# Optimization experiments

Hardware: AMD Instinct MI355X
Metric: run time of the kernel (lower is better)

Reference implementation:

```python
import jax, jax.numpy as jnp
import numpy as np

H = 128
W = 128
DELTA = 7000.0  # sigmainv in the original (delta default 7000)


def setup_inputs() -> dict:
    key = jax.random.key(0)
    k1, k2, k3, k4 = jax.random.split(key, 4)
    B, P, F, TH, TW = 2, 300, 512, 512, 512
    points_bxpx3 = jax.random.uniform(k1, (B, P, 3), jnp.float32) * 2.0 - 1.0  # NDC cube [-1,1]
    faces_fx3 = jax.random.randint(k2, (F, 3), 0, P, dtype=jnp.int32)
    uv_bxpx2 = jax.random.uniform(k3, (B, P, 2), jnp.float32)  # texcoords in [0,1]
    texture_bx3xthxtw = jax.random.uniform(k4, (B, 3, TH, TW), jnp.float32)
    return {"points_bxpx3": points_bxpx3, "faces_fx3": faces_fx3,
            "uv_bxpx2": uv_bxpx2, "texture_bx3xthxtw": texture_bx3xthxtw}


def _edge(ax, ay, bx, by, px, py):
    # signed area * 2 of triangle (a, b, p); standard edge function
    return (bx - ax) * (py - ay) - (by - ay) * (px - ax)


def _seg_d2(ax, ay, bx, by, px, py):
    # squared distance from point p to segment (a, b)
    abx, aby = bx - ax, by - ay
    apx, apy = px - ax, py - ay
    denom = abx * abx + aby * aby + 1e-12
    t = jnp.clip((apx * abx + apy * aby) / denom, 0.0, 1.0)
    dx = apx - t * abx
    dy = apy - t * aby
    return dx * dx + dy * dy


def _rasterize(points_bxpx3, faces_fx3, feats_bxfx3xd, height, width, delta):
    """Soft DIB-R-style rasterizer.
    Returns (imfeat [B,H,W,D], improb [B,H,W,1]).
    """
    B = points_bxpx3.shape[0]
    v = points_bxpx3[:, faces_fx3]                      # (B,F,3,3) gathered face vertices
    x0, x1, x2 = (v[:, :, i, 0][:, :, None, None] for i in range(3))
    y0, y1, y2 = (v[:, :, i, 1][:, :, None, None] for i in range(3))
    z0, z1, z2 = (v[:, :, i, 2][:, :, None, None] for i in range(3))

    # pixel-center grid in NDC; y flipped (top row = +1)
    px = ((jnp.arange(width, dtype=points_bxpx3.dtype) + 0.5) / width * 2.0 - 1.0)[None, None, None, :]
    py = (1.0 - (jnp.arange(height, dtype=points_bxpx3.dtype) + 0.5) / height * 2.0)[None, None, :, None]

    area = _edge(x0, y0, x1, y1, x2, y2)                # (B,F,1,1) == normal_z (cross-product z)
    front = area > 1e-8                                  # front-facing (normalz > 0) cull
    inv_area = 1.0 / jnp.where(front, area, 1.0)

    w0 = _edge(x1, y1, x2, y2, px, py) * inv_area        # (B,F,H,W) barycentrics
    w1 = _edge(x2, y2, x0, y0, px, py) * inv_area
    w2 = _edge(x0, y0, x1, y1, px, py) * inv_area
    inside = front & (w0 >= 0) & (w1 >= 0) & (w2 >= 0)

    z_pix = w0 * z0 + w1 * z1 + w2 * z2                  # interpolated depth
    zbuf = jnp.where(inside, z_pix, -1e9)
    best = jnp.argmax(zbuf, axis=1)                      # (B,H,W) nearest covering face
    hit = jnp.any(inside, axis=1)[..., None].astype(points_bxpx3.dtype)  # (B,H,W,1)

    # gather winning barycentrics and per-face vertex features
    w = jnp.stack([w0, w1, w2], axis=-1)                 # (B,F,H,W,3)
    idx = jnp.broadcast_to(best[:, None, :, :, None], (B, 1, height, width, 3))
    wb = jnp.take_along_axis(w, idx, axis=1)[:, 0]       # (B,H,W,3)
    fb = jax.vmap(lambda f, i: f[i])(feats_bxfx3xd, best)  # (B,H,W,3,D)
    imfeat = jnp.einsum('bhwk,bhwkd->bhwd', wb, fb) * hit

    # soft coverage: prob of each face = exp(-delta * d2(pixel, triangle)); z-buffer blend
    d2 = jnp.minimum(
        jnp.minimum(_seg_d2(x0, y0, x1, y1, px, py), _seg_d2(x1, y1, x2, y2, px, py)),
        _seg_d2(x2, y2, x0, y0, px, py))
    d2 = jnp.where(inside, 0.0, d2)
    p = jnp.where(front, jnp.exp(-delta * d2), 0.0)      # (B,F,H,W)
    log_miss = jnp.sum(jnp.log1p(-jnp.clip(p, 0.0, 1.0 - 1e-7)), axis=1)  # (B,H,W)
    improb = (1.0 - jnp.exp(log_miss))[..., None]
    return imfeat, improb


def _fragmentshader(imtexcoords, texture_bx3xthxtw, hardmask):
    # bilinear texture sampling; background is zero
    B, C, TH, TW = texture_bx3xthxtw.shape
    u = jnp.clip(imtexcoords[..., 0], 0.0, 1.0)
    vv = jnp.clip(imtexcoords[..., 1], 0.0, 1.0)
    fx = u * (TW - 1)
    fy = (1.0 - vv) * (TH - 1)
    x0 = jnp.floor(fx).astype(jnp.int32); x1 = jnp.minimum(x0 + 1, TW - 1)
    y0 = jnp.floor(fy).astype(jnp.int32); y1 = jnp.minimum(y0 + 1, TH - 1)
    wx = (fx - x0)[:, None]; wy = (fy - y0)[:, None]     # (B,1,H,W)

    def g(tex, yy, xx):  # tex (C,TH,TW), yy/xx (H,W) -> (C,H,W)
        return tex[:, yy, xx]
    c00 = jax.vmap(g)(texture_bx3xthxtw, y0, x0)
    c01 = jax.vmap(g)(texture_bx3xthxtw, y0, x1)
    c10 = jax.vmap(g)(texture_bx3xthxtw, y1, x0)
    c11 = jax.vmap(g)(texture_bx3xthxtw, y1, x1)
    col = (c00 * (1 - wx) * (1 - wy) + c01 * wx * (1 - wy)
           + c10 * (1 - wx) * wy + c11 * wx * wy)        # (B,C,H,W)
    return col.transpose(0, 2, 3, 1) * hardmask          # (B,H,W,C)


def reference(points_bxpx3, faces_fx3, uv_bxpx2, texture_bx3xthxtw):
    # texture mode: per-face vertex features = [u, v, mask=1]
    uvf = uv_bxpx2[:, faces_fx3]                          # (B,F,3,2)
    ones = jnp.ones_like(uvf[..., :1])
    feats = jnp.concatenate([uvf, ones], axis=-1)         # (B,F,3,3)
    imfeat, improb = _rasterize(points_bxpx3, faces_fx3, feats, H, W, DELTA)
    imtexcoords = imfeat[..., :2]
    hardmask = jax.lax.stop_gradient(imfeat[..., 2:3])    # .detach() in the original
    imrender = _fragmentshader(imtexcoords, texture_bx3xthxtw, hardmask)
    return imrender, improb
```

## Files before the change

### kernel.cpp

```cpp
#include <hip/hip_runtime.h>
#include <math.h>

constexpr int kB = 2, kP = 300, kF = 512, kH = 128, kW = 128, kTH = 512, kTW = 512;
constexpr float kDelta = 7000.0f;
constexpr float kCut = 0.0363f;
constexpr float kThr2 = 0.012928f;
constexpr float kLogInside = -15.9423847f;

__device__ __forceinline__ unsigned zmap(float f) {
    unsigned b = __float_as_uint(f);
    return (b & 0x80000000u) ? ~b : (b | 0x80000000u);
}

__global__ __launch_bounds__(512, 8) void render_all(const float* __restrict__ pts,
                                                     const int* __restrict__ faces,
                                                     const float* __restrict__ uvs,
                                                     const float* __restrict__ tex,
                                                     float* __restrict__ out) {
    __shared__ float4 sA[kF], sB[kF], sC[kF];
    __shared__ float4 sV[kF];
    __shared__ ushort4 s_j3[kF];
    __shared__ float s_uv[kP * 2];
    __shared__ unsigned long long s_best[64];
    __shared__ float s_lm[64];
    __shared__ int s_wsum[8];
    float4* s_pxW = sA;
    int4* s_pxO = (int4*)(sA + 64);

    int tile = (int)blockIdx.x;
    int b = tile >> 8;
    int rem = tile & 255;
    int ty = rem >> 4, tx = rem & 15;
    int tid = (int)threadIdx.x;
    int lane = tid & 63;
    int wv = tid >> 6;

    {
        int f = tid;
        int i0 = faces[f * 3 + 0], i1 = faces[f * 3 + 1], i2 = faces[f * 3 + 2];
        const float* pb = pts + b * kP * 3;
        float x0 = pb[i0 * 3], y0 = pb[i0 * 3 + 1], z0 = pb[i0 * 3 + 2];
        float x1 = pb[i1 * 3], y1 = pb[i1 * 3 + 1], z1 = pb[i1 * 3 + 2];
        float x2 = pb[i2 * 3], y2 = pb[i2 * 3 + 1], z2 = pb[i2 * 3 + 2];
        float area = (x1 - x0) * (y2 - y0) - (y1 - y0) * (x2 - x0);
        bool front = area > 1e-8f;

        const float* gu = uvs + b * (kP * 2);
        for (int i = tid; i < kP * 2; i += 512) s_uv[i] = gu[i];
        if (tid < 64) { s_best[tid] = 0ull; s_lm[tid] = 0.0f; }
        sA[f] = make_float4(0.0f, 0.0f, -1e30f, 0.0f);
        sB[f] = make_float4(0.0f, -1e30f, 0.0f, 0.0f);
        sC[f] = make_float4(-1e30f, 0.0f, 0.0f, 0.0f);
        sV[f] = make_float4(1e15f, 1e15f, 1e15f, 1e15f);
        unsigned long long bal = __ballot(front);
        if (lane == 0) s_wsum[wv] = __popcll(bal);
        __syncthreads();

        int base = 0;
#pragma unroll
        for (int w = 0; w < 8; ++w) base += (w < wv) ? s_wsum[w] : 0;
        int k = base + __popcll(bal & ((1ull << lane) - 1ull));

        if (front) {
            int slot = ((k & 7) << 6) | (k >> 3);
            float inv_a = 1.0f / area;
            float e0x = x2 - x1, e0y = y2 - y1;
            float e1x = x0 - x2, e1y = y0 - y2;
            float e2x = x1 - x0, e2y = y1 - y0;
            float l0 = fmaf(e0x, e0x, e0y * e0y);
            float l1 = fmaf(e1x, e1x, e1y * e1y);
            float l2 = fmaf(e2x, e2x, e2y * e2y);
            float s0 = rsqrtf(l0 + 1e-12f);
            float s1 = rsqrtf(l1 + 1e-12f);
            float s2 = rsqrtf(l2 + 1e-12f);
            float A0 = -e0y * s0, B0 = e0x * s0, C0 = (e0y * x1 - e0x * y1) * s0;
            float A1 = -e1y * s1, B1 = e1x * s1, C1 = (e1y * x2 - e1x * y2) * s1;
            float A2 = -e2y * s2, B2 = e2x * s2, C2 = (e2y * x0 - e2x * y0) * s2;
            float a0 = -e0y * inv_a, b0 = e0x * inv_a, c0 = (e0y * x1 - e0x * y1) * inv_a;
            float a1 = -e1y * inv_a, b1 = e1x * inv_a, c1 = (e1y * x2 - e1x * y2) * inv_a;
            float a2 = -e2y * inv_a, b2 = e2x * inv_a, c2 = (e2y * x0 - e2x * y0) * inv_a;
            sA[slot] = make_float4(A0, B0, C0, A1);
            sB[slot] = make_float4(B1, C1, A2, B2);
            sC[slot] = make_float4(C2,
                                   a0 * z0 + a1 * z1 + a2 * z2,
                                   b0 * z0 + b1 * z1 + b2 * z2,
                                   c0 * z0 + c1 * z1 + c2 * z2);
            sV[slot] = make_float4(x0, y0, x1, y1);
            s_j3[slot] = make_ushort4((unsigned short)i0, (unsigned short)i1,
                                      (unsigned short)i2, 0);
        }
    }
    __syncthreads();

    int pyi = ty * 8 + (lane >> 3);
    int pxi = tx * 8 + (lane & 7);
    float px = ((float)pxi + 0.5f) * (2.0f / 128.0f) - 1.0f;
    float py = 1.0f - ((float)pyi + 0.5f) * (2.0f / 128.0f);

    float cx = (float)(tx * 8 + 4) * (2.0f / 128.0f) - 1.0f;
    float cy = 1.0f - (float)(ty * 8 + 4) * (2.0f / 128.0f);
    unsigned long long m;
    {
        int slt = (wv << 6) + lane;
        float4 a4 = sA[slt];
        float4 b4 = sB[slt];
        float4 c4 = sC[slt];
        float4 vv = sV[slt];
        float L0 = fmaf(a4.x, cx, fmaf(a4.y, cy, a4.z));
        float L1 = fmaf(a4.w, cx, fmaf(b4.x, cy, b4.y));
        float L2 = fmaf(b4.z, cx, fmaf(b4.w, cy, c4.x));
        float minc = fminf(fminf(L0, L1), L2);
        float D = fmaf(a4.x, b4.x, -a4.w * a4.y);
        float rD = __builtin_amdgcn_rcpf(D);
        float v2x = (a4.y * b4.y - b4.x * a4.z) * rD;
        float v2y = (a4.w * a4.z - a4.x * b4.y) * rD;
        float e0x = v2x - vv.z, e0y = v2y - vv.w;
        float e1x = vv.x - v2x, e1y = vv.y - v2y;
        float e2x = vv.z - vv.x, e2y = vv.w - vv.y;
        float p0x = cx - vv.x, p0y = cy - vv.y;
        float p1x = cx - vv.z, p1y = cy - vv.w;
        float p2x = cx - v2x, p2y = cy - v2y;
        float dot0 = fmaf(p1x, e0x, p1y * e0y), len0 = fmaf(e0x, e0x, e0y * e0y);
        float dot1 = fmaf(p2x, e1x, p2y * e1y), len1 = fmaf(e1x, e1x, e1y * e1y);
        float dot2 = fmaf(p0x, e2x, p0y * e2y), len2 = fmaf(e2x, e2x, e2y * e2y);
        float c0 = (dot0 >= 0.0f && dot0 <= len0) ? L0 * L0 : 1e30f;
        float c1 = (dot1 >= 0.0f && dot1 <= len1) ? L1 * L1 : 1e30f;
        float c2 = (dot2 >= 0.0f && dot2 <= len2) ? L2 * L2 : 1e30f;
        float dv0 = fmaf(p0x, p0x, p0y * p0y);
        float dv1 = fmaf(p1x, p1x, p1y * p1y);
        float dv2 = fmaf(p2x, p2x, p2y * p2y);
        float d2c = fminf(fminf(fminf(c0, c1), fminf(c2, dv0)), fminf(dv1, dv2));
        bool admit = (minc >= 0.0f) | (d2c <= kThr2);
        m = __ballot(admit);
    }

    float bestz = -1e9f;
    int besti = -1, icnt = 0;
    float lm = 0.0f;

    while (m) {
        int l = (int)__builtin_ctzll(m);
        m &= (m - 1);
        int fs = (wv << 6) + l;
        int k = (l << 3) | wv;
        float4 h0 = sA[fs];
        float4 h1 = sB[fs];
        float4 h2 = sC[fs];
        float L0 = fmaf(h0.x, px, fmaf(h0.y, py, h0.z));
        float L1 = fmaf(h0.w, px, fmaf(h1.x, py, h1.y));
        float L2 = fmaf(h1.z, px, fmaf(h1.w, py, h2.x));
        float minL = fminf(fminf(L0, L1), L2);
        bool inside = minL >= 0.0f;
        float z = fmaf(h2.y, px, fmaf(h2.z, py, h2.w));
        if (inside && z > bestz) { bestz = z; besti = k; }
        icnt += inside ? 1 : 0;
        float db = fminf(fminf(fabsf(L0), fabsf(L1)), fabsf(L2));
        bool need = (!inside) & (db < kCut);
        if (__any(need)) {
            float4 vv = sV[fs];
            float D = fmaf(h0.x, h1.x, -h0.w * h0.y);
            float rD = __builtin_amdgcn_rcpf(D);
            float v2x = (h0.y * h1.y - h1.x * h0.z) * rD;
            float v2y = (h0.w * h0.z - h0.x * h1.y) * rD;
            float e0x = v2x - vv.z, e0y = v2y - vv.w;
            float e1x = vv.x - v2x, e1y = vv.y - v2y;
            float e2x = vv.z - vv.x, e2y = vv.w - vv.y;
            float p0x = px - vv.x, p0y = py - vv.y;
            float p1x = px - vv.z, p1y = py - vv.w;
            float p2x = px - v2x, p2y = py - v2y;
            float dot0 = fmaf(p1x, e0x, p1y * e0y), len0 = fmaf(e0x, e0x, e0y * e0y);
            float dot1 = fmaf(p2x, e1x, p2y * e1y), len1 = fmaf(e1x, e1x, e1y * e1y);
            float dot2 = fmaf(p0x, e2x, p0y * e2y), len2 = fmaf(e2x, e2x, e2y * e2y);
            float c0 = (dot0 >= 0.0f && dot0 <= len0) ? L0 * L0 : 1e30f;
            float c1 = (dot1 >= 0.0f && dot1 <= len1) ? L1 * L1 : 1e30f;
            float c2 = (dot2 >= 0.0f && dot2 <= len2) ? L2 * L2 : 1e30f;
            float dv0 = fmaf(p0x, p0x, p0y * p0y);
            float dv1 = fmaf(p1x, p1x, p1y * p1y);
            float dv2 = fmaf(p2x, p2x, p2y * p2y);
            float d2 = fminf(fminf(fminf(c0, c1), fminf(c2, dv0)), fminf(dv1, dv2));
            float p = __expf(-kDelta * d2);
            p = fminf(p, 1.0f - 1e-7f);
            float lp = __logf(1.0f - p);
            lm += need ? lp : 0.0f;
        }
    }
    lm = fmaf((float)icnt, kLogInside, lm);

    if (besti >= 0) {
        unsigned long long key = ((unsigned long long)zmap(bestz) << 32) |
                                 (unsigned long long)(511 - besti);
        atomicMax(&s_best[lane], key);
    }
    atomicAdd(&s_lm[lane], lm);
    __syncthreads();

    if (tid < 64) {
        unsigned long long key = s_best[tid];
        float improb = 1.0f - expf(s_lm[tid]);
        float u = 0.0f, v = 0.0f, mk = 0.0f;
        if (key != 0ull) {
            int bi = 511 - (int)(key & 0xFFFFFFFFull);
            int slot = ((bi & 7) << 6) | (bi >> 3);
            float4 vv = sV[slot];
            float4 h0 = sA[slot];
            float4 h1 = sB[slot];
            float D = fmaf(h0.x, h1.x, -h0.w * h0.y);
            float rD = __builtin_amdgcn_rcpf(D);
            float v2x = (h0.y * h1.y - h1.x * h0.z) * rD;
            float v2y = (h0.w * h0.z - h0.x * h1.y) * rD;
            float x0 = vv.x, y0 = vv.y, x1 = vv.z, y1 = vv.w;
            float area = (x1 - x0) * (v2y - y0) - (y1 - y0) * (v2x - x0);
            float inv_a = 1.0f / area;
            float w0 = ((v2x - x1) * (py - y1) - (v2y - y1) * (px - x1)) * inv_a;
            float w1 = ((x0 - v2x) * (py - v2y) - (y0 - v2y) * (px - v2x)) * inv_a;
            float w2 = ((x1 - x0) * (py - y0) - (y1 - y0) * (px - x0)) * inv_a;
            ushort4 j = s_j3[slot];
            u = w0 * s_uv[j.x * 2] + w1 * s_uv[j.y * 2] + w2 * s_uv[j.z * 2];
            v = w0 * s_uv[j.x * 2 + 1] + w1 * s_uv[j.y * 2 + 1] + w2 * s_uv[j.z * 2 + 1];
            mk = w0 + w1 + w2;
        }
        float uc = fminf(fmaxf(u, 0.0f), 1.0f);
        float vc = fminf(fmaxf(v, 0.0f), 1.0f);
        float fx = uc * (float)(kTW - 1);
        float fy = (1.0f - vc) * (float)(kTH - 1);
        int xi0 = (int)floorf(fx), yi0 = (int)floorf(fy);
        int xi1 = min(xi0 + 1, kTW - 1), yi1 = min(yi0 + 1, kTH - 1);
        float wx = fx - (float)xi0, wy = fy - (float)yi0;
        float w00 = (1.0f - wx) * (1.0f - wy) * mk;
        float w01 = wx * (1.0f - wy) * mk;
        float w10 = (1.0f - wx) * wy * mk;
        float w11 = wx * wy * mk;
        s_pxW[tid] = make_float4(w00, w01, w10, w11);
        s_pxO[tid] = make_int4(yi0 * kTW + xi0, yi0 * kTW + xi1,
                               yi1 * kTW + xi0, yi1 * kTW + xi1);
        out[kB * kH * kW * 3 + (b * kH + pyi) * kW + pxi] = improb;
    }
    __syncthreads();

    if (tid < 192) {
        int pix = tid & 63;
        int c = tid >> 6;
        float4 w = s_pxW[pix];
        int4 o = s_pxO[pix];
        const float* tc = tex + ((size_t)b * 3 + c) * kTH * kTW;
        float col = tc[o.x] * w.x + tc[o.y] * w.y + tc[o.z] * w.z + tc[o.w] * w.w;
        int qy = ty * 8 + (pix >> 3);
        int qx = tx * 8 + (pix & 7);
        out[((b * kH + qy) * kW + qx) * 3 + c] = col;
    }
}

extern "C" void kernel_launch(void* const* d_in, const int* in_sizes, int n_in,
                              void* d_out, int out_size, void* d_ws, size_t ws_size,
                              hipStream_t stream) {
    const float* pts = (const float*)d_in[0];
    const int* faces = (const int*)d_in[1];
    const float* uvs = (const float*)d_in[2];
    const float* tex = (const float*)d_in[3];
    float* out = (float*)d_out;
    render_all<<<kB * 256, 512, 0, stream>>>(pts, faces, uvs, tex, out);
}
```

Before: 18.35 us.

## Precompute per-face segment planes and UV planes; fast path for tile-interior faces

```diff
diff --git a/kernel.cpp b/kernel.cpp
--- a/kernel.cpp
+++ b/kernel.cpp
@@ -5,6 +5,7 @@
 constexpr float kDelta = 7000.0f;
 constexpr float kCut = 0.0363f;
 constexpr float kThr2 = 0.012928f;
+constexpr float kIntThr = 0.0785f;
 constexpr float kLogInside = -15.9423847f;
 
 __device__ __forceinline__ unsigned zmap(float f) {
@@ -12,20 +13,17 @@
     return (b & 0x80000000u) ? ~b : (b | 0x80000000u);
 }
 
-__global__ __launch_bounds__(512, 8) void render_all(const float* __restrict__ pts,
+__global__ __launch_bounds__(512, 4) void render_all(const float* __restrict__ pts,
                                                      const int* __restrict__ faces,
                                                      const float* __restrict__ uvs,
                                                      const float* __restrict__ tex,
                                                      float* __restrict__ out) {
-    __shared__ float4 sA[kF], sB[kF], sC[kF];
-    __shared__ float4 sV[kF];
-    __shared__ ushort4 s_j3[kF];
-    __shared__ float s_uv[kP * 2];
+    __shared__ float4 sF[8][kF];
     __shared__ unsigned long long s_best[64];
     __shared__ float s_lm[64];
     __shared__ int s_wsum[8];
-    float4* s_pxW = sA;
-    int4* s_pxO = (int4*)(sA + 64);
+    float4* s_pxW = sF[0];
+    int4* s_pxO = (int4*)(sF[0] + 64);
 
     int tile = (int)blockIdx.x;
     int b = tile >> 8;
@@ -42,16 +40,17 @@
         float x0 = pb[i0 * 3], y0 = pb[i0 * 3 + 1], z0 = pb[i0 * 3 + 2];
         float x1 = pb[i1 * 3], y1 = pb[i1 * 3 + 1], z1 = pb[i1 * 3 + 2];
         float x2 = pb[i2 * 3], y2 = pb[i2 * 3 + 1], z2 = pb[i2 * 3 + 2];
+        const float* ub = uvs + b * (kP * 2);
+        float u0 = ub[i0 * 2], vv0 = ub[i0 * 2 + 1];
+        float u1 = ub[i1 * 2], vv1 = ub[i1 * 2 + 1];
+        float u2 = ub[i2 * 2], vv2 = ub[i2 * 2 + 1];
         float area = (x1 - x0) * (y2 - y0) - (y1 - y0) * (x2 - x0);
         bool front = area > 1e-8f;
 
-        const float* gu = uvs + b * (kP * 2);
-        for (int i = tid; i < kP * 2; i += 512) s_uv[i] = gu[i];
         if (tid < 64) { s_best[tid] = 0ull; s_lm[tid] = 0.0f; }
-        sA[f] = make_float4(0.0f, 0.0f, -1e30f, 0.0f);
-        sB[f] = make_float4(0.0f, -1e30f, 0.0f, 0.0f);
-        sC[f] = make_float4(-1e30f, 0.0f, 0.0f, 0.0f);
-        sV[f] = make_float4(1e15f, 1e15f, 1e15f, 1e15f);
+        sF[0][f] = make_float4(0.0f, 0.0f, -1e30f, 0.0f);
+        sF[1][f] = make_float4(0.0f, -1e30f, 0.0f, 0.0f);
+        sF[2][f] = make_float4(-1e30f, 0.0f, 0.0f, 0.0f);
         unsigned long long bal = __ballot(front);
         if (lane == 0) s_wsum[wv] = __popcll(bal);
         __syncthreads();
@@ -79,15 +78,24 @@
             float a0 = -e0y * inv_a, b0 = e0x * inv_a, c0 = (e0y * x1 - e0x * y1) * inv_a;
             float a1 = -e1y * inv_a, b1 = e1x * inv_a, c1 = (e1y * x2 - e1x * y2) * inv_a;
             float a2 = -e2y * inv_a, b2 = e2x * inv_a, c2 = (e2y * x0 - e2x * y0) * inv_a;
-            sA[slot] = make_float4(A0, B0, C0, A1);
-            sB[slot] = make_float4(B1, C1, A2, B2);
-            sC[slot] = make_float4(C2,
-                                   a0 * z0 + a1 * z1 + a2 * z2,
-                                   b0 * z0 + b1 * z1 + b2 * z2,
-                                   c0 * z0 + c1 * z1 + c2 * z2);
-            sV[slot] = make_float4(x0, y0, x1, y1);
-            s_j3[slot] = make_ushort4((unsigned short)i0, (unsigned short)i1,
-                                      (unsigned short)i2, 0);
+            sF[0][slot] = make_float4(A0, B0, C0, A1);
+            sF[1][slot] = make_float4(B1, C1, A2, B2);
+            sF[2][slot] = make_float4(C2,
+                                      a0 * z0 + a1 * z1 + a2 * z2,
+                                      b0 * z0 + b1 * z1 + b2 * z2,
+                                      c0 * z0 + c1 * z1 + c2 * z2);
+            sF[3][slot] = make_float4(e0x * s0, e0y * s0,
+                                      -(e0x * x1 + e0y * y1) * s0, l0 * s0);
+            sF[4][slot] = make_float4(e1x * s1, e1y * s1,
+                                      -(e1x * x2 + e1y * y2) * s1, l1 * s1);
+            sF[5][slot] = make_float4(e2x * s2, e2y * s2,
+                                      -(e2x * x0 + e2y * y0) * s2, l2 * s2);
+            sF[6][slot] = make_float4(a0 * u0 + a1 * u1 + a2 * u2,
+                                      b0 * u0 + b1 * u1 + b2 * u2,
+                                      c0 * u0 + c1 * u1 + c2 * u2, 0.0f);
+            sF[7][slot] = make_float4(a0 * vv0 + a1 * vv1 + a2 * vv2,
+                                      b0 * vv0 + b1 * vv1 + b2 * vv2,
+                                      c0 * vv0 + c1 * vv1 + c2 * vv2, 0.0f);
         }
     }
     __syncthreads();
@@ -99,84 +107,83 @@
 
     float cx = (float)(tx * 8 + 4) * (2.0f / 128.0f) - 1.0f;
     float cy = 1.0f - (float)(ty * 8 + 4) * (2.0f / 128.0f);
-    unsigned long long m;
+    unsigned long long me, mi;
     {
         int slt = (wv << 6) + lane;
-        float4 a4 = sA[slt];
-        float4 b4 = sB[slt];
-        float4 c4 = sC[slt];
-        float4 vv = sV[slt];
+        float4 a4 = sF[0][slt];
+        float4 b4 = sF[1][slt];
+        float4 c4 = sF[2][slt];
+        float4 t0 = sF[3][slt];
+        float4 t1 = sF[4][slt];
+        float4 t2 = sF[5][slt];
         float L0 = fmaf(a4.x, cx, fmaf(a4.y, cy, a4.z));
         float L1 = fmaf(a4.w, cx, fmaf(b4.x, cy, b4.y));
         float L2 = fmaf(b4.z, cx, fmaf(b4.w, cy, c4.x));
         float minc = fminf(fminf(L0, L1), L2);
-        float D = fmaf(a4.x, b4.x, -a4.w * a4.y);
-        float rD = __builtin_amdgcn_rcpf(D);
-        float v2x = (a4.y * b4.y - b4.x * a4.z) * rD;
-        float v2y = (a4.w * a4.z - a4.x * b4.y) * rD;
-        float e0x = v2x - vv.z, e0y = v2y - vv.w;
-        float e1x = vv.x - v2x, e1y = vv.y - v2y;
-        float e2x = vv.z - vv.x, e2y = vv.w - vv.y;
-        float p0x = cx - vv.x, p0y = cy - vv.y;
-        float p1x = cx - vv.z, p1y = cy - vv.w;
-        float p2x = cx - v2x, p2y = cy - v2y;
-        float dot0 = fmaf(p1x, e0x, p1y * e0y), len0 = fmaf(e0x, e0x, e0y * e0y);
-        float dot1 = fmaf(p2x, e1x, p2y * e1y), len1 = fmaf(e1x, e1x, e1y * e1y);
-        float dot2 = fmaf(p0x, e2x, p0y * e2y), len2 = fmaf(e2x, e2x, e2y * e2y);
-        float c0 = (dot0 >= 0.0f && dot0 <= len0) ? L0 * L0 : 1e30f;
-        float c1 = (dot1 >= 0.0f && dot1 <= len1) ? L1 * L1 : 1e30f;
-        float c2 = (dot2 >= 0.0f && dot2 <= len2) ? L2 * L2 : 1e30f;
-        float dv0 = fmaf(p0x, p0x, p0y * p0y);
-        float dv1 = fmaf(p1x, p1x, p1y * p1y);
-        float dv2 = fmaf(p2x, p2x, p2y * p2y);
+        float s0 = fmaf(t0.x, cx, fmaf(t0.y, cy, t0.z));
+        float s1 = fmaf(t1.x, cx, fmaf(t1.y, cy, t1.z));
+        float s2 = fmaf(t2.x, cx, fmaf(t2.y, cy, t2.z));
+        float q0 = L0 * L0, q1 = L1 * L1, q2 = L2 * L2;
+        float c0 = (s0 >= 0.0f && s0 <= t0.w) ? q0 : 1e30f;
+        float c1 = (s1 >= 0.0f && s1 <= t1.w) ? q1 : 1e30f;
+        float c2 = (s2 >= 0.0f && s2 <= t2.w) ? q2 : 1e30f;
+        float dv1 = fmaf(s0, s0, q0);
+        float dv2 = fmaf(s1, s1, q1);
+        float dv0 = fmaf(s2, s2, q2);
         float d2c = fminf(fminf(fminf(c0, c1), fminf(c2, dv0)), fminf(dv1, dv2));
+        bool inter = minc >= kIntThr;
         bool admit = (minc >= 0.0f) | (d2c <= kThr2);
-        m = __ballot(admit);
+        mi = __ballot(inter);
+        me = __ballot(admit && !inter);
     }
 
     float bestz = -1e9f;
-    int besti = -1, icnt = 0;
+    int besti = 1 << 30, icnt = 0;
     float lm = 0.0f;
 
-    while (m) {
-        int l = (int)__builtin_ctzll(m);
-        m &= (m - 1);
+    icnt += (int)__popcll(mi);
+    while (mi) {
+        int l = (int)__builtin_ctzll(mi);
+        mi &= (mi - 1);
         int fs = (wv << 6) + l;
         int k = (l << 3) | wv;
-        float4 h0 = sA[fs];
-        float4 h1 = sB[fs];
-        float4 h2 = sC[fs];
+        float4 h2 = sF[2][fs];
+        float z = fmaf(h2.y, px, fmaf(h2.z, py, h2.w));
+        if (z > bestz || (z == bestz && k < besti)) { bestz = z; besti = k; }
+    }
+
+    while (me) {
+        int l = (int)__builtin_ctzll(me);
+        me &= (me - 1);
+        int fs = (wv << 6) + l;
+        int k = (l << 3) | wv;
+        float4 h0 = sF[0][fs];
+        float4 h1 = sF[1][fs];
+        float4 h2 = sF[2][fs];
         float L0 = fmaf(h0.x, px, fmaf(h0.y, py, h0.z));
         float L1 = fmaf(h0.w, px, fmaf(h1.x, py, h1.y));
         float L2 = fmaf(h1.z, px, fmaf(h1.w, py, h2.x));
         float minL = fminf(fminf(L0, L1), L2);
         bool inside = minL >= 0.0f;
         float z = fmaf(h2.y, px, fmaf(h2.z, py, h2.w));
-        if (inside && z > bestz) { bestz = z; besti = k; }
+        if (inside && (z > bestz || (z == bestz && k < besti))) { bestz = z; besti = k; }
         icnt += inside ? 1 : 0;
         float db = fminf(fminf(fabsf(L0), fabsf(L1)), fabsf(L2));
         bool need = (!inside) & (db < kCut);
         if (__any(need)) {
-            float4 vv = sV[fs];
-            float D = fmaf(h0.x, h1.x, -h0.w * h0.y);
-            float rD = __builtin_amdgcn_rcpf(D);
-            float v2x = (h0.y * h1.y - h1.x * h0.z) * rD;
-            float v2y = (h0.w * h0.z - h0.x * h1.y) * rD;
-            float e0x = v2x - vv.z, e0y = v2y - vv.w;
-            float e1x = vv.x - v2x, e1y = vv.y - v2y;
-            float e2x = vv.z - vv.x, e2y = vv.w - vv.y;
-            float p0x = px - vv.x, p0y = py - vv.y;
-            float p1x = px - vv.z, p1y = py - vv.w;
-            float p2x = px - v2x, p2y = py - v2y;
-            float dot0 = fmaf(p1x, e0x, p1y * e0y), len0 = fmaf(e0x, e0x, e0y * e0y);
-            float dot1 = fmaf(p2x, e1x, p2y * e1y), len1 = fmaf(e1x, e1x, e1y * e1y);
-            float dot2 = fmaf(p0x, e2x, p0y * e2y), len2 = fmaf(e2x, e2x, e2y * e2y);
-            float c0 = (dot0 >= 0.0f && dot0 <= len0) ? L0 * L0 : 1e30f;
-            float c1 = (dot1 >= 0.0f && dot1 <= len1) ? L1 * L1 : 1e30f;
-            float c2 = (dot2 >= 0.0f && dot2 <= len2) ? L2 * L2 : 1e30f;
-            float dv0 = fmaf(p0x, p0x, p0y * p0y);
-            float dv1 = fmaf(p1x, p1x, p1y * p1y);
-            float dv2 = fmaf(p2x, p2x, p2y * p2y);
+            float4 t0 = sF[3][fs];
+            float4 t1 = sF[4][fs];
+            float4 t2 = sF[5][fs];
+            float s0 = fmaf(t0.x, px, fmaf(t0.y, py, t0.z));
+            float s1 = fmaf(t1.x, px, fmaf(t1.y, py, t1.z));
+            float s2 = fmaf(t2.x, px, fmaf(t2.y, py, t2.z));
+            float q0 = L0 * L0, q1 = L1 * L1, q2 = L2 * L2;
+            float c0 = (s0 >= 0.0f && s0 <= t0.w) ? q0 : 1e30f;
+            float c1 = (s1 >= 0.0f && s1 <= t1.w) ? q1 : 1e30f;
+            float c2 = (s2 >= 0.0f && s2 <= t2.w) ? q2 : 1e30f;
+            float dv1 = fmaf(s0, s0, q0);
+            float dv2 = fmaf(s1, s1, q1);
+            float dv0 = fmaf(s2, s2, q2);
             float d2 = fminf(fminf(fminf(c0, c1), fminf(c2, dv0)), fminf(dv1, dv2));
             float p = __expf(-kDelta * d2);
             p = fminf(p, 1.0f - 1e-7f);
@@ -186,7 +193,7 @@
     }
     lm = fmaf((float)icnt, kLogInside, lm);
 
-    if (besti >= 0) {
+    if (besti < (1 << 30)) {
         unsigned long long key = ((unsigned long long)zmap(bestz) << 32) |
                                  (unsigned long long)(511 - besti);
         atomicMax(&s_best[lane], key);
@@ -201,23 +208,11 @@
         if (key != 0ull) {
             int bi = 511 - (int)(key & 0xFFFFFFFFull);
             int slot = ((bi & 7) << 6) | (bi >> 3);
-            float4 vv = sV[slot];
-            float4 h0 = sA[slot];
-            float4 h1 = sB[slot];
-            float D = fmaf(h0.x, h1.x, -h0.w * h0.y);
-            float rD = __builtin_amdgcn_rcpf(D);
-            float v2x = (h0.y * h1.y - h1.x * h0.z) * rD;
-            float v2y = (h0.w * h0.z - h0.x * h1.y) * rD;
-            float x0 = vv.x, y0 = vv.y, x1 = vv.z, y1 = vv.w;
-            float area = (x1 - x0) * (v2y - y0) - (y1 - y0) * (v2x - x0);
-            float inv_a = 1.0f / area;
-            float w0 = ((v2x - x1) * (py - y1) - (v2y - y1) * (px - x1)) * inv_a;
-            float w1 = ((x0 - v2x) * (py - v2y) - (y0 - v2y) * (px - v2x)) * inv_a;
-            float w2 = ((x1 - x0) * (py - y0) - (y1 - y0) * (px - x0)) * inv_a;
-            ushort4 j = s_j3[slot];
-            u = w0 * s_uv[j.x * 2] + w1 * s_uv[j.y * 2] + w2 * s_uv[j.z * 2];
-            v = w0 * s_uv[j.x * 2 + 1] + w1 * s_uv[j.y * 2 + 1] + w2 * s_uv[j.z * 2 + 1];
-            mk = w0 + w1 + w2;
+            float4 uq = sF[6][slot];
+            float4 vq = sF[7][slot];
+            u = fmaf(uq.x, px, fmaf(uq.y, py, uq.z));
+            v = fmaf(vq.x, px, fmaf(vq.y, py, vq.z));
+            mk = 1.0f;
         }
         float uc = fminf(fmaxf(u, 0.0f), 1.0f);
         float vc = fminf(fmaxf(v, 0.0f), 1.0f);
```

Result: faster. 17.64 us (-3.9%).
